# Performance work log

Hardware: AMD Instinct MI355X
Metric: run time of the kernel (lower is better)

The kernel has to match this reference:

```python
import jax, jax.numpy as jnp
import numpy as np

N = 100000   # nodes per type
E = 500000   # edges per edge type
HID = 128    # hidden_channels
H = 4        # heads
D = HID // H # head dim = 32
L = 2        # layers
T = 2        # node types: 0=user, 1=item
R = 2        # edge types: 0=user->item, 1=item->user


def setup_inputs() -> dict:
    key = jax.random.key(0)
    ks = jax.random.split(key, 16)
    s = jnp.float32(0.05)
    f32 = jnp.float32
    return {
        "x_user": jax.random.normal(ks[0], (N, HID), f32),
        "x_item": jax.random.normal(ks[1], (N, HID), f32),
        "W_in": jax.random.normal(ks[2], (T, HID, HID), f32) * s,
        "b_in": jnp.zeros((T, HID), f32),
        "Wk": jax.random.normal(ks[3], (L, T, HID, HID), f32) * s,
        "bk": jnp.zeros((L, T, HID), f32),
        "Wq": jax.random.normal(ks[4], (L, T, HID, HID), f32) * s,
        "bq": jnp.zeros((L, T, HID), f32),
        "Wv": jax.random.normal(ks[5], (L, T, HID, HID), f32) * s,
        "bv": jnp.zeros((L, T, HID), f32),
        "a_rel": jax.random.normal(ks[6], (L, R, H, D, D), f32) * s,
        "m_rel": jax.random.normal(ks[7], (L, R, H, D, D), f32) * s,
        "p_rel": jnp.ones((L, R, H), f32),
        "Wo": jax.random.normal(ks[8], (L, T, HID, HID), f32) * s,
        "bo": jnp.zeros((L, T, HID), f32),
        "skip": jnp.zeros((L, T), f32),
        "edge_ui": jax.random.randint(ks[9], (2, E), 0, N, dtype=jnp.int32),
        "edge_iu": jax.random.randint(ks[10], (2, E), 0, N, dtype=jnp.int32),
    }


def _seg_softmax(logits, seg, n):
    # numerically stable softmax over edges grouped by destination node
    m = jax.ops.segment_max(logits, seg, num_segments=n)            # [N,H]
    m = jnp.where(jnp.isfinite(m), m, jnp.float32(0.0))
    e = jnp.exp(logits - m[seg])                                    # [E,H]
    z = jax.ops.segment_sum(e, seg, num_segments=n)                 # [N,H]
    return e / (z[seg] + jnp.float32(1e-16))


def reference(x_user, x_item, W_in, b_in, Wk, bk, Wq, bq, Wv, bv,
              a_rel, m_rel, p_rel, Wo, bo, skip, edge_ui, edge_iu):
    scale = jnp.float32(1.0 / np.sqrt(D))
    # per-node-type input linear + relu (lin_dict)
    h = [jax.nn.relu(x_user @ W_in[0] + b_in[0]),
         jax.nn.relu(x_item @ W_in[1] + b_in[1])]
    # (edge_type_id, src_type, dst_type, edge_index)
    etypes = [(0, 0, 1, edge_ui), (1, 1, 0, edge_iu)]
    for l in range(L):
        k = [(h[t] @ Wk[l, t] + bk[l, t]).reshape(N, H, D) for t in range(T)]
        q = [(h[t] @ Wq[l, t] + bq[l, t]).reshape(N, H, D) for t in range(T)]
        v = [(h[t] @ Wv[l, t] + bv[l, t]).reshape(N, H, D) for t in range(T)]
        agg = [jnp.zeros((N, H, D), h[0].dtype) for _ in range(T)]
        for r, st, dt, e in etypes:
            src, dst = e[0], e[1]
            # relation-specific transforms applied on node table (N < E)
            k_r = jnp.einsum('nhd,hde->nhe', k[st], a_rel[l, r])
            v_r = jnp.einsum('nhd,hde->nhe', v[st], m_rel[l, r])
            logits = jnp.sum(q[dt][dst] * k_r[src], axis=-1) * p_rel[l, r] * scale  # [E,H]
            alpha = _seg_softmax(logits, dst, N)                                    # [E,H]
            msg = alpha[:, :, None] * v_r[src]                                      # [E,H,D]
            agg[dt] = agg[dt] + jax.ops.segment_sum(msg, dst, num_segments=N)
        h_new = []
        for t in range(T):
            out = agg[t].reshape(N, HID)
            a = jax.nn.gelu(out, approximate=False) @ Wo[l, t] + bo[l, t]
            beta = jax.nn.sigmoid(skip[l, t])
            hn = beta * a + (1.0 - beta) * h[t]
            if l > 0:  # model-level residual (i > 0 in torch code)
                hn = hn + h[t]
            h_new.append(hn)
        h = h_new
    return jnp.stack(h)  # [T, N, HID]
```

## Files before the change

kernel.cpp:

```cpp
#include <hip/hip_runtime.h>
#include <stdint.h>
#include <stdio.h>

#define NN 100000
#define NE 500000
#define HID 128
#define NH 4
#define HD 32
#define LL 2
#define SCANB 1024
#define NB ((NN + SCANB - 1) / SCANB)

typedef unsigned short u16;
typedef unsigned char u8;
typedef unsigned int u32;
typedef __attribute__((ext_vector_type(8))) short bfrag;
typedef __attribute__((ext_vector_type(4))) float f32x4;
typedef __attribute__((ext_vector_type(2))) float f32x2;

__device__ __forceinline__ float b2f(u32 lo16) {
  union { u32 u; float f; } c; c.u = lo16; return c.f;
}
__device__ __forceinline__ u16 f2b(float f) {
  union { float f; u32 u; } c; c.f = f;
  u32 u = c.u;
  u32 r = (u + 0x7FFFu + ((u >> 16) & 1u)) >> 16;
  return (u16)r;
}
__device__ __forceinline__ float geluf(float x) {
  return 0.5f * x * (1.0f + erff(x * 0.70710678118654752f));
}
__device__ __forceinline__ void up8(uint4 a, float* f) {
  f[0] = b2f(a.x << 16); f[1] = b2f(a.x & 0xFFFF0000u);
  f[2] = b2f(a.y << 16); f[3] = b2f(a.y & 0xFFFF0000u);
  f[4] = b2f(a.z << 16); f[5] = b2f(a.z & 0xFFFF0000u);
  f[6] = b2f(a.w << 16); f[7] = b2f(a.w & 0xFFFF0000u);
}
__device__ __forceinline__ float dot32(uint4 a, uint4 b, const float* qv) {
  u32 w[8] = {a.x, a.y, a.z, a.w, b.x, b.y, b.z, b.w};
  float s = 0.f;
#pragma unroll
  for (int j = 0; j < 8; ++j) {
    f32x2 p0 = __builtin_amdgcn_cvt_pk_f32_fp8(w[j], false);
    f32x2 p1 = __builtin_amdgcn_cvt_pk_f32_fp8(w[j], true);
    s += qv[4 * j] * p0.x + qv[4 * j + 1] * p0.y + qv[4 * j + 2] * p1.x + qv[4 * j + 3] * p1.y;
  }
  return s;
}
__device__ __forceinline__ void acc32(uint4 a, uint4 b, float ev, float* acc) {
  u32 w[8] = {a.x, a.y, a.z, a.w, b.x, b.y, b.z, b.w};
#pragma unroll
  for (int j = 0; j < 8; ++j) {
    f32x2 p0 = __builtin_amdgcn_cvt_pk_f32_fp8(w[j], false);
    f32x2 p1 = __builtin_amdgcn_cvt_pk_f32_fp8(w[j], true);
    acc[4 * j] += ev * p0.x; acc[4 * j + 1] += ev * p0.y;
    acc[4 * j + 2] += ev * p1.x; acc[4 * j + 3] += ev * p1.y;
  }
}

__global__ __launch_bounds__(256) void csr_count(const int* __restrict__ e0,
                                                 const int* __restrict__ e1,
                                                 int* __restrict__ deg,
                                                 int* __restrict__ hist) {
  if (blockIdx.x == 0 && blockIdx.y == 0 && threadIdx.x < 128) hist[threadIdx.x] = 0;
  int r = blockIdx.y;
  const int* edges = r ? e1 : e0;
  int e = blockIdx.x * 256 + threadIdx.x;
  if (e < NE) atomicAdd(&deg[(size_t)r * NN + edges[NE + e]], 1);
}

__global__ __launch_bounds__(SCANB) void scan1(const int* __restrict__ deg,
                                               int* __restrict__ rp,
                                               int* __restrict__ bsum,
                                               int* __restrict__ hist) {
  __shared__ int ls[SCANB];
  __shared__ int lh[64];
  int r = blockIdx.y;
  int t = threadIdx.x;
  int g = blockIdx.x * SCANB + t;
  int v = (g < NN) ? deg[(size_t)r * NN + g] : 0;
  ls[t] = v;
  if (t < 64) lh[t] = 0;
  __syncthreads();
  if (g < NN) atomicAdd(&lh[v < 63 ? v : 63], 1);
#pragma unroll
  for (int off = 1; off < SCANB; off <<= 1) {
    int u = (t >= off) ? ls[t - off] : 0;
    __syncthreads();
    ls[t] += u;
    __syncthreads();
  }
  if (g < NN) rp[(size_t)r * (NN + 1) + g] = ls[t] - v;
  if (t == SCANB - 1) bsum[r * NB + blockIdx.x] = ls[t];
  if (t < 64 && lh[t]) atomicAdd(&hist[r * 64 + t], lh[t]);
}

__global__ __launch_bounds__(128) void scan2(const int* __restrict__ bsum,
                                             int* __restrict__ boff,
                                             const int* __restrict__ hist,
                                             int* __restrict__ hcur) {
  __shared__ int ls[128];
  int r = blockIdx.y;
  int t = threadIdx.x;
  int v = (t < NB) ? bsum[r * NB + t] : 0;
  ls[t] = v;
  __syncthreads();
#pragma unroll
  for (int off = 1; off < 128; off <<= 1) {
    int u = (t >= off) ? ls[t - off] : 0;
    __syncthreads();
    ls[t] += u;
    __syncthreads();
  }
  if (t < NB) boff[r * NB + t] = ls[t] - v;
  __syncthreads();
  int hv = (t < 64) ? hist[r * 64 + t] : 0;
  ls[t] = hv;
  __syncthreads();
#pragma unroll
  for (int off = 1; off < 64; off <<= 1) {
    int u = (t >= off) ? ls[t - off] : 0;
    __syncthreads();
    ls[t] += u;
    __syncthreads();
  }
  if (t < 64) hcur[r * 64 + t] = ls[t] - hv;
}

__global__ __launch_bounds__(SCANB) void scan3(int* __restrict__ rp,
                                               int* __restrict__ cursor,
                                               const int* __restrict__ boff,
                                               const int* __restrict__ deg,
                                               int* __restrict__ hcur,
                                               int* __restrict__ o0,
                                               int* __restrict__ o1) {
  __shared__ int lh[64];
  __shared__ int lbase[64];
  int r = blockIdx.y;
  int* order = r ? o1 : o0;
  int t = threadIdx.x;
  int g = blockIdx.x * SCANB + t;
  if (t < 64) lh[t] = 0;
  int dg = 0;
  if (g < NN) {
    int v = rp[(size_t)r * (NN + 1) + g] + boff[r * NB + blockIdx.x];
    rp[(size_t)r * (NN + 1) + g] = v;
    cursor[(size_t)r * NN + g] = v;
    dg = deg[(size_t)r * NN + g];
    if (dg > 63) dg = 63;
  }
  if (g == 0) rp[(size_t)r * (NN + 1) + NN] = NE;
  __syncthreads();
  int rank = 0;
  if (g < NN) rank = atomicAdd(&lh[dg], 1);
  __syncthreads();
  if (t < 64)
    lbase[t] = lh[t] ? atomicAdd(&hcur[r * 64 + t], lh[t]) : 0;
  __syncthreads();
  if (g < NN) order[lbase[dg] + rank] = g;
}

__global__ __launch_bounds__(256) void csr_fill(const int* __restrict__ e0,
                                                const int* __restrict__ e1,
                                                int* __restrict__ cursor,
                                                int* __restrict__ s0,
                                                int* __restrict__ s1) {
  int r = blockIdx.y;
  const int* edges = r ? e1 : e0;
  int* srcs = r ? s1 : s0;
  int e = blockIdx.x * 256 + threadIdx.x;
  if (e < NE) {
    int pos = atomicAdd(&cursor[(size_t)r * NN + edges[NE + e]], 1);
    srcs[pos] = edges[e];
  }
}

__global__ __launch_bounds__(256) void prep_all(
    const float* __restrict__ W_in,
    const float* __restrict__ Wo,
    const float* __restrict__ Wq, const float* __restrict__ bq,
    const float* __restrict__ Wk, const float* __restrict__ bk,
    const float* __restrict__ Wv, const float* __restrict__ bv,
    const float* __restrict__ a_rel, const float* __restrict__ m_rel,
    const float* __restrict__ p_rel,
    u16* __restrict__ winT, u16* __restrict__ woT,
    u16* __restrict__ wqkvT, float* __restrict__ bqkv) {
  const float scale = 0.17677669529663687f;
  int y = blockIdx.y;
  int idx = blockIdx.x * 256 + threadIdx.x;
  if (y < 10) {
    const float* src; u16* dst;
    const float* bsrc = nullptr; float* bdst = nullptr;
    bool useP = false; int m = 0;
    if (y < 2) {
      m = y; src = W_in + (size_t)m * HID * HID; dst = winT + (size_t)m * HID * HID;
    } else if (y < 6) {
      m = y - 2; src = Wo + (size_t)m * HID * HID; dst = woT + (size_t)m * HID * HID;
    } else {
      m = y - 6; src = Wq + (size_t)m * HID * HID;
      dst = wqkvT + (size_t)m * 3 * HID * HID;
      useP = true; bsrc = bq + (size_t)m * HID; bdst = bqkv + (size_t)m * 3 * HID;
    }
    int k = idx >> 7, n = idx & 127;
    float v = src[idx];
    if (useP) {
      int l = m >> 1, t = m & 1;
      v *= p_rel[((l << 1) | (1 - t)) * NH + (n >> 5)] * scale;
    }
    dst[(size_t)n * HID + k] = f2b(v);
    if (bdst != nullptr && blockIdx.x == 0 && threadIdx.x < HID) {
      int col = threadIdx.x;
      int l = m >> 1, t = m & 1;
      bdst[col] = bsrc[col] * p_rel[((l << 1) | (1 - t)) * NH + (col >> 5)] * scale;
    }
  } else {
    int c = y - 10;
    int l = c >> 2, t = (c >> 1) & 1, which = c & 1;
    const float* W  = (which == 0 ? Wk : Wv) + (size_t)(l * 2 + t) * HID * HID;
    const float* b  = (which == 0 ? bk : bv) + (size_t)(l * 2 + t) * HID;
    const float* Ar = (which == 0 ? a_rel : m_rel) + (size_t)(l * 2 + t) * NH * HD * HD;
    u16* Wd = wqkvT + ((size_t)(l * 2 + t) * 3 + 1 + which) * HID * HID;
    float* bd = bqkv + ((size_t)(l * 2 + t) * 3 + 1 + which) * HID;
    int i = idx >> 7, col = idx & 127;
    int h = col >> 5, e = col & 31;
    {
      const float* ap = Ar + h * HD * HD + e;
      const float* wp = W + (size_t)i * HID + h * HD;
      float s = 0.f;
#pragma unroll
      for (int d = 0; d < HD; ++d) s += wp[d] * ap[d * HD];
      Wd[(size_t)col * HID + i] = f2b(s);
    }
    if (blockIdx.x == 0 && threadIdx.x < HID) {
      int col2 = threadIdx.x, h2 = col2 >> 5, e2 = col2 & 31;
      const float* ap = Ar + h2 * HD * HD + e2;
      const float* bp = b + h2 * HD;
      float s = 0.f;
#pragma unroll
      for (int d = 0; d < HD; ++d) s += bp[d] * ap[d * HD];
      bd[col2] = s;
    }
  }
}

__global__ __launch_bounds__(256) void qkv_gemm(
    const u16* __restrict__ h0, const u16* __restrict__ h1,
    const u16* __restrict__ WT,
    const float* __restrict__ bias,
    u16* __restrict__ q0, u16* __restrict__ q1,
    u8* __restrict__ k0, u8* __restrict__ k1,
    u8* __restrict__ v0, u8* __restrict__ v1, int gb) {
  __shared__ __align__(16) u16 sW[2][HID * HID];
  const int t = blockIdx.x >= gb;
  const int bx = t ? blockIdx.x - gb : blockIdx.x;
  const u16* A = t ? h1 : h0;
  const u16* Wg = WT + (size_t)t * 3 * HID * HID;
  const float* bs = bias + (size_t)t * 3 * HID;
  u16* Oq = t ? q1 : q0;
  u8* Ok = t ? k1 : k0;
  u8* Ov = t ? v1 : v0;

  const int lane = threadIdx.x & 63;
  const int wid = threadIdx.x >> 6;
  const int l16 = lane & 15, g = lane >> 4;
  const int rbase = bx * 128 + wid * 32;

  auto stageW = [&](int m, int buf) {
    const u16* Wm = Wg + (size_t)m * HID * HID;
#pragma unroll
    for (int j = 0; j < 8; ++j) {
      int ins = wid * 8 + j;
      int o16 = ins * 64 + lane;
      int row = o16 >> 4, ch = o16 & 15;
      const u16* src = Wm + (size_t)row * HID + ((ch ^ (row & 7)) << 3);
      u16* dst = &sW[buf][0] + (size_t)ins * 512;
      __builtin_amdgcn_global_load_lds(
          (const __attribute__((address_space(1))) unsigned int*)src,
          (__attribute__((address_space(3))) unsigned int*)dst, 16, 0, 0);
    }
  };

  bfrag af[2][4];
#pragma unroll
  for (int rt = 0; rt < 2; ++rt) {
    int row = rbase + rt * 16 + l16;
    int rl = row < NN ? row : NN - 1;
    const bfrag* ap = (const bfrag*)(A + (size_t)rl * HID);
#pragma unroll
    for (int ks = 0; ks < 4; ++ks) af[rt][ks] = ap[ks * 4 + g];
  }

  stageW(0, 0);
  __syncthreads();

  const int rr = threadIdx.x >> 1, half = threadIdx.x & 1;
  const int grow = bx * 128 + rr;

#pragma unroll
  for (int m = 0; m < 3; ++m) {
    if (m + 1 < 3) stageW(m + 1, (m + 1) & 1);
    f32x4 acc[2][8];
#pragma unroll
    for (int rt = 0; rt < 2; ++rt)
#pragma unroll
      for (int ct = 0; ct < 8; ++ct) acc[rt][ct] = (f32x4){0.f, 0.f, 0.f, 0.f};
#pragma unroll
    for (int ct = 0; ct < 8; ++ct) {
      int row = ct * 16 + l16;
      bfrag wf[4];
#pragma unroll
      for (int ks = 0; ks < 4; ++ks)
        wf[ks] = *(const bfrag*)&sW[m & 1][(size_t)row * HID +
                                           (((ks * 4 + g) ^ (row & 7)) << 3)];
#pragma unroll
      for (int ks = 0; ks < 4; ++ks)
#pragma unroll
        for (int rt = 0; rt < 2; ++rt)
          acc[rt][ct] = __builtin_amdgcn_mfma_f32_16x16x32_bf16(wf[ks], af[rt][ks],
                                                                acc[rt][ct], 0, 0, 0);
    }
    __syncthreads();
    u16* tile = &sW[m & 1][0];
    u8* t8 = (u8*)tile;
#pragma unroll
    for (int rt = 0; rt < 2; ++rt) {
      int r = wid * 32 + rt * 16 + l16;
#pragma unroll
      for (int ct = 0; ct < 8; ++ct) {
        int nc = ct * 16 + g * 4;
        const float4 bb = *(const float4*)(bs + m * HID + nc);
        float o0 = acc[rt][ct][0] + bb.x;
        float o1 = acc[rt][ct][1] + bb.y;
        float o2 = acc[rt][ct][2] + bb.z;
        float o3 = acc[rt][ct][3] + bb.w;
        if (m == 0) {
          u32 lo = (u32)f2b(o0) | ((u32)f2b(o1) << 16);
          u32 hi = (u32)f2b(o2) | ((u32)f2b(o3) << 16);
          int sg = ((nc >> 3) ^ (r & 7));
          *(uint2*)&tile[(size_t)r * HID + sg * 8 + (nc & 7)] = make_uint2(lo, hi);
        } else {
          u32 pk = __builtin_amdgcn_cvt_pk_fp8_f32(o0, o1, 0u, false);
          pk = __builtin_amdgcn_cvt_pk_fp8_f32(o2, o3, pk, true);
          int sg = ((nc >> 4) ^ (r & 7));
          *(u32*)&t8[(size_t)r * HID + sg * 16 + (nc & 15)] = pk;
        }
      }
    }
    __syncthreads();
    if (grow < NN) {
      if (m == 0) {
#pragma unroll
        for (int i = 0; i < 8; ++i) {
          int gg = half * 8 + i;
          uint4 d = *(const uint4*)&tile[(size_t)rr * HID + ((gg ^ (rr & 7)) * 8)];
          *(uint4*)(Oq + (size_t)grow * HID + gg * 8) = d;
        }
      } else {
        u8* O8 = (m == 1) ? Ok : Ov;
#pragma unroll
        for (int i = 0; i < 4; ++i) {
          int gg = half * 4 + i;
          uint4 d = *(const uint4*)&t8[(size_t)rr * HID + ((gg ^ (rr & 7)) * 16)];
          *(uint4*)(O8 + (size_t)grow * HID + gg * 16) = d;
        }
      }
    }
    if (m + 1 < 3) __syncthreads();
  }
}

template <int NMAT, bool RELU, bool SKIP, bool FP8KV, bool AF32>
__global__ __launch_bounds__(256) void mfgemm(
    const void* __restrict__ A0, const void* __restrict__ A1, int M, int gb,
    const u16* __restrict__ WT, size_t wtStride,
    const float* __restrict__ bias, size_t biasStride,
    u16* __restrict__ O00, u16* __restrict__ O01, u16* __restrict__ O02,
    u16* __restrict__ O10, u16* __restrict__ O11, u16* __restrict__ O12,
    float* __restrict__ Of0, float* __restrict__ Of1,
    const u16* __restrict__ hp0, const u16* __restrict__ hp1,
    const float* __restrict__ skipP, int resflag) {
  __shared__ __align__(16) u16 sW[HID * HID];
  const int t = blockIdx.x >= gb;
  const int bx = t ? blockIdx.x - gb : blockIdx.x;
  const void* A = t ? A1 : A0;
  const u16* Wg = WT + (size_t)t * wtStride;
  const float* bs = bias + (size_t)t * biasStride;
  u16* Ob = t ? O10 : O00;
  float* Of = t ? Of1 : Of0;
  const u16* hprev = t ? hp1 : hp0;

  const int lane = threadIdx.x & 63;
  const int wid = threadIdx.x >> 6;
  const int l16 = lane & 15, g = lane >> 4;
  const int rbase = bx * 128 + wid * 32;

  float beta = 0.f;
  if (SKIP) beta = 1.f / (1.f + __expf(-skipP[t]));

  {
    const u16* Wm = Wg;
#pragma unroll
    for (int j = 0; j < 8; ++j) {
      int ins = wid * 8 + j;
      int o16 = ins * 64 + lane;
      int row = o16 >> 4, ch = o16 & 15;
      const u16* src = Wm + (size_t)row * HID + ((ch ^ (row & 7)) << 3);
      u16* dst = sW + (size_t)ins * 512;
      __builtin_amdgcn_global_load_lds(
          (const __attribute__((address_space(1))) unsigned int*)src,
          (__attribute__((address_space(3))) unsigned int*)dst, 16, 0, 0);
    }
  }

  bfrag af[2][4];
  int rowA[2];
#pragma unroll
  for (int rt = 0; rt < 2; ++rt) {
    int row = rbase + rt * 16 + l16;
    rowA[rt] = row;
    int rl = row < M ? row : M - 1;
    if (AF32) {
      const float* apf = (const float*)A + (size_t)rl * HID;
#pragma unroll
      for (int ks = 0; ks < 4; ++ks) {
        float4 u0 = *(const float4*)(apf + (ks * 4 + g) * 8);
        float4 u1 = *(const float4*)(apf + (ks * 4 + g) * 8 + 4);
        union { u16 s[8]; bfrag b; } pk;
        pk.s[0] = f2b(u0.x); pk.s[1] = f2b(u0.y); pk.s[2] = f2b(u0.z); pk.s[3] = f2b(u0.w);
        pk.s[4] = f2b(u1.x); pk.s[5] = f2b(u1.y); pk.s[6] = f2b(u1.z); pk.s[7] = f2b(u1.w);
        af[rt][ks] = pk.b;
      }
    } else {
      const bfrag* ap = (const bfrag*)A + (size_t)rl * (HID / 8);
#pragma unroll
      for (int ks = 0; ks < 4; ++ks) af[rt][ks] = ap[ks * 4 + g];
    }
  }

  __syncthreads();

  f32x4 acc[2][8];
#pragma unroll
  for (int rt = 0; rt < 2; ++rt)
#pragma unroll
    for (int ct = 0; ct < 8; ++ct) acc[rt][ct] = (f32x4){0.f, 0.f, 0.f, 0.f};
#pragma unroll
  for (int ct = 0; ct < 8; ++ct) {
    int row = ct * 16 + l16;
    bfrag wf[4];
#pragma unroll
    for (int ks = 0; ks < 4; ++ks)
      wf[ks] = *(const bfrag*)&sW[(size_t)row * HID + (((ks * 4 + g) ^ (row & 7)) << 3)];
#pragma unroll
    for (int ks = 0; ks < 4; ++ks)
#pragma unroll
      for (int rt = 0; rt < 2; ++rt)
        acc[rt][ct] = __builtin_amdgcn_mfma_f32_16x16x32_bf16(wf[ks], af[rt][ks],
                                                              acc[rt][ct], 0, 0, 0);
  }

  if (Ob != nullptr) {
    __syncthreads();
#pragma unroll
    for (int rt = 0; rt < 2; ++rt) {
      int r = wid * 32 + rt * 16 + l16;
      int row = rowA[rt];
      int rl = row < M ? row : M - 1;
#pragma unroll
      for (int ct = 0; ct < 8; ++ct) {
        int nc = ct * 16 + g * 4;
        const float4 bb = *(const float4*)(bs + nc);
        float o0 = acc[rt][ct][0] + bb.x;
        float o1 = acc[rt][ct][1] + bb.y;
        float o2 = acc[rt][ct][2] + bb.z;
        float o3 = acc[rt][ct][3] + bb.w;
        if (RELU) {
          o0 = fmaxf(o0, 0.f); o1 = fmaxf(o1, 0.f);
          o2 = fmaxf(o2, 0.f); o3 = fmaxf(o3, 0.f);
        }
        if (SKIP) {
          uint2 hh2 = *(const uint2*)(hprev + (size_t)rl * HID + nc);
          float h0 = b2f(hh2.x << 16), h1 = b2f(hh2.x & 0xFFFF0000u);
          float h2 = b2f(hh2.y << 16), h3 = b2f(hh2.y & 0xFFFF0000u);
          o0 = beta * o0 + (1.f - beta) * h0;
          o1 = beta * o1 + (1.f - beta) * h1;
          o2 = beta * o2 + (1.f - beta) * h2;
          o3 = beta * o3 + (1.f - beta) * h3;
          if (resflag) { o0 += h0; o1 += h1; o2 += h2; o3 += h3; }
        }
        u32 lo = (u32)f2b(o0) | ((u32)f2b(o1) << 16);
        u32 hi = (u32)f2b(o2) | ((u32)f2b(o3) << 16);
        int sg = ((nc >> 3) ^ (r & 7));
        *(uint2*)&sW[(size_t)r * HID + sg * 8 + (nc & 7)] = make_uint2(lo, hi);
      }
    }
    __syncthreads();
    int rr = threadIdx.x >> 1, half = threadIdx.x & 1;
    int grow = bx * 128 + rr;
    if (grow < M) {
#pragma unroll
      for (int i = 0; i < 8; ++i) {
        int gg = half * 8 + i;
        uint4 d = *(const uint4*)&sW[(size_t)rr * HID + ((gg ^ (rr & 7)) * 8)];
        *(uint4*)(Ob + (size_t)grow * HID + gg * 8) = d;
      }
    }
  } else {
#pragma unroll
    for (int rt = 0; rt < 2; ++rt) {
      int row = rowA[rt];
      if (row >= M) continue;
#pragma unroll
      for (int ct = 0; ct < 8; ++ct) {
        int nc = ct * 16 + g * 4;
        const float4 bb = *(const float4*)(bs + nc);
        float o0 = acc[rt][ct][0] + bb.x;
        float o1 = acc[rt][ct][1] + bb.y;
        float o2 = acc[rt][ct][2] + bb.z;
        float o3 = acc[rt][ct][3] + bb.w;
        if (RELU) {
          o0 = fmaxf(o0, 0.f); o1 = fmaxf(o1, 0.f);
          o2 = fmaxf(o2, 0.f); o3 = fmaxf(o3, 0.f);
        }
        if (SKIP) {
          uint2 hh2 = *(const uint2*)(hprev + (size_t)row * HID + nc);
          float h0 = b2f(hh2.x << 16), h1 = b2f(hh2.x & 0xFFFF0000u);
          float h2 = b2f(hh2.y << 16), h3 = b2f(hh2.y & 0xFFFF0000u);
          o0 = beta * o0 + (1.f - beta) * h0;
          o1 = beta * o1 + (1.f - beta) * h1;
          o2 = beta * o2 + (1.f - beta) * h2;
          o3 = beta * o3 + (1.f - beta) * h3;
          if (resflag) { o0 += h0; o1 += h1; o2 += h2; o3 += h3; }
        }
        *(float4*)(Of + (size_t)row * HID + nc) = make_float4(o0, o1, o2, o3);
      }
    }
  }
}

__global__ __launch_bounds__(256) void agg_csr(
    const int* __restrict__ rp0, const int* __restrict__ ss0, const int* __restrict__ od0,
    const u16* __restrict__ q0, const u8* __restrict__ k0,
    const u8* __restrict__ v0, u16* __restrict__ o0,
    const int* __restrict__ rp1, const int* __restrict__ ss1, const int* __restrict__ od1,
    const u16* __restrict__ q1, const u8* __restrict__ k1,
    const u8* __restrict__ v1, u16* __restrict__ o1, int agb) {
  const int r = blockIdx.x >= agb;
  const int bx = r ? blockIdx.x - agb : blockIdx.x;
  int i = bx * 256 + threadIdx.x;
  if (i >= NN * NH) return;
  const int* rowptr = r ? rp1 : rp0;
  const int* srcs = r ? ss1 : ss0;
  const int* order = r ? od1 : od0;
  const u16* qT = r ? q1 : q0;
  const u8* kT = r ? k1 : k0;
  const u8* vT = r ? v1 : v0;
  u16* aggb = r ? o1 : o0;

  int dst = order[i >> 2], h = i & 3;
  float qv[HD];
  {
    const uint4* qp = (const uint4*)(qT + (size_t)dst * HID + h * HD);
#pragma unroll
    for (int j = 0; j < 4; ++j) up8(qp[j], qv + j * 8);
  }
  float acc[HD];
#pragma unroll
  for (int j = 0; j < HD; ++j) acc[j] = 0.f;
  float z = 0.f;
  int b = rowptr[dst], e2 = rowptr[dst + 1];
  int idx = b;
  for (; idx + 2 <= e2; idx += 2) {
    int s0 = srcs[idx], s1 = srcs[idx + 1];
    const uint4* kp0 = (const uint4*)(kT + (size_t)s0 * HID + h * HD);
    const uint4* vp0 = (const uint4*)(vT + (size_t)s0 * HID + h * HD);
    const uint4* kp1 = (const uint4*)(kT + (size_t)s1 * HID + h * HD);
    const uint4* vp1 = (const uint4*)(vT + (size_t)s1 * HID + h * HD);
    uint4 kA = kp0[0], kB = kp0[1];
    uint4 kC = kp1[0], kD = kp1[1];
    uint4 vA = vp0[0], vB = vp0[1];
    uint4 vC = vp1[0], vD = vp1[1];
    float d0 = dot32(kA, kB, qv);
    float d1 = dot32(kC, kD, qv);
    float ev0 = __expf(fminf(d0, 60.f));
    float ev1 = __expf(fminf(d1, 60.f));
    z += ev0 + ev1;
    acc32(vA, vB, ev0, acc);
    acc32(vC, vD, ev1, acc);
  }
  if (idx < e2) {
    int s0 = srcs[idx];
    const uint4* kp0 = (const uint4*)(kT + (size_t)s0 * HID + h * HD);
    const uint4* vp0 = (const uint4*)(vT + (size_t)s0 * HID + h * HD);
    uint4 kA = kp0[0], kB = kp0[1];
    uint4 vA = vp0[0], vB = vp0[1];
    float d0 = dot32(kA, kB, qv);
    float ev0 = __expf(fminf(d0, 60.f));
    z += ev0;
    acc32(vA, vB, ev0, acc);
  }
  float inv = 1.f / (z + 1e-16f);
  u16* ap = aggb + (size_t)dst * HID + h * HD;
  u32 w[16];
#pragma unroll
  for (int j = 0; j < 16; ++j) {
    float a0 = geluf(acc[2 * j] * inv);
    float a1 = geluf(acc[2 * j + 1] * inv);
    w[j] = (u32)f2b(a0) | ((u32)f2b(a1) << 16);
  }
#pragma unroll
  for (int j = 0; j < 4; ++j)
    *(uint4*)(ap + j * 8) = make_uint4(w[4 * j], w[4 * j + 1], w[4 * j + 2], w[4 * j + 3]);
}

extern "C" void kernel_launch(void* const* d_in, const int* in_sizes, int n_in,
                              void* d_out, int out_size, void* d_ws, size_t ws_size,
                              hipStream_t stream) {
  const float* x_user = (const float*)d_in[0];
  const float* x_item = (const float*)d_in[1];
  const float* W_in = (const float*)d_in[2];
  const float* b_in = (const float*)d_in[3];
  const float* Wk = (const float*)d_in[4];
  const float* bk = (const float*)d_in[5];
  const float* Wq = (const float*)d_in[6];
  const float* bq = (const float*)d_in[7];
  const float* Wv = (const float*)d_in[8];
  const float* bv = (const float*)d_in[9];
  const float* a_rel = (const float*)d_in[10];
  const float* m_rel = (const float*)d_in[11];
  const float* p_rel = (const float*)d_in[12];
  const float* Wo = (const float*)d_in[13];
  const float* bo = (const float*)d_in[14];
  const float* skipP = (const float*)d_in[15];
  const int* edge_ui = (const int*)d_in[16];
  const int* edge_iu = (const int*)d_in[17];
  float* out = (float*)d_out;

  char* p = (char*)d_ws;
  auto take = [&](size_t bytes) {
    void* r = (void*)p;
    p += (bytes + 255) & ~(size_t)255;
    return r;
  };
  size_t nodeB = (size_t)NN * HID * sizeof(u16);
  size_t node8 = (size_t)NN * HID;
  u16* hb[2] = {(u16*)take(nodeB), (u16*)take(nodeB)};
  u16* qb[2] = {(u16*)take(nodeB), (u16*)take(nodeB)};
  u8* kb[2] = {(u8*)take(node8), (u8*)take(node8)};
  u8* vb[2] = {(u8*)take(node8), (u8*)take(node8)};
  u16* aggb[2] = {(u16*)take(nodeB), (u16*)take(nodeB)};
  int* deg2   = (int*)take((size_t)2 * NN * 4);
  int* cur2   = (int*)take((size_t)2 * NN * 4);
  int* bsum2  = (int*)take((size_t)2 * NB * 4);
  int* boff2  = (int*)take((size_t)2 * NB * 4);
  int* hist2  = (int*)take((size_t)2 * 64 * 4);
  int* hcur2  = (int*)take((size_t)2 * 64 * 4);
  int* rp2    = (int*)take((size_t)2 * (NN + 1) * 4);
  int* srcs[2]  = {(int*)take((size_t)NE * 4), (int*)take((size_t)NE * 4)};
  int* order[2] = {(int*)take((size_t)NN * 4), (int*)take((size_t)NN * 4)};
  u16* winT  = (u16*)take((size_t)2 * HID * HID * 2);
  u16* woT   = (u16*)take((size_t)4 * HID * HID * 2);
  u16* wqkvT = (u16*)take((size_t)2 * 2 * 3 * HID * HID * 2);
  float* bqkv = (float*)take((size_t)2 * 2 * 3 * HID * 4);
  size_t used = (size_t)(p - (char*)d_ws);
  if (used > ws_size) {
    fprintf(stderr, "HGT kernel: workspace too small: need %zu, have %zu\n", used, ws_size);
    return;
  }

  const int GB = (NN + 127) / 128;
  const int EB = (NE + 255) / 256;
  dim3 blk(256);

  hipMemsetAsync(deg2, 0, (size_t)2 * NN * 4, stream);
  prep_all<<<dim3(64, 18), blk, 0, stream>>>(W_in, Wo, Wq, bq, Wk, bk, Wv, bv,
                                             a_rel, m_rel, p_rel,
                                             winT, woT, wqkvT, bqkv);
  csr_count<<<dim3(EB, 2), blk, 0, stream>>>(edge_ui, edge_iu, deg2, hist2);
  scan1<<<dim3(NB, 2), SCANB, 0, stream>>>(deg2, rp2, bsum2, hist2);
  scan2<<<dim3(1, 2), 128, 0, stream>>>(bsum2, boff2, hist2, hcur2);
  scan3<<<dim3(NB, 2), SCANB, 0, stream>>>(rp2, cur2, boff2, deg2, hcur2,
                                           order[0], order[1]);
  csr_fill<<<dim3(EB, 2), blk, 0, stream>>>(edge_ui, edge_iu, cur2, srcs[0], srcs[1]);
  int* rowptr[2] = {rp2, rp2 + (NN + 1)};

  mfgemm<1, true, false, false, true><<<2 * GB, blk, 0, stream>>>(
      x_user, x_item, NN, GB, winT, HID * HID, b_in, HID,
      hb[0], nullptr, nullptr, hb[1], nullptr, nullptr,
      nullptr, nullptr, nullptr, nullptr, nullptr, 0);

  const int AGB = (NN * NH + 255) / 256;
  for (int l = 0; l < LL; ++l) {
    qkv_gemm<<<2 * GB, blk, 0, stream>>>(
        hb[0], hb[1],
        wqkvT + (size_t)l * 2 * 3 * HID * HID,
        bqkv + (size_t)l * 2 * 3 * HID,
        qb[0], qb[1], kb[0], kb[1], vb[0], vb[1], GB);
    agg_csr<<<2 * AGB, blk, 0, stream>>>(
        rowptr[0], srcs[0], order[0], qb[1], kb[0], vb[0], aggb[1],
        rowptr[1], srcs[1], order[1], qb[0], kb[1], vb[1], aggb[0], AGB);
    if (l == 0) {
      mfgemm<1, false, true, false, false><<<2 * GB, blk, 0, stream>>>(
          aggb[0], aggb[1], NN, GB,
          woT, HID * HID, bo, HID,
          hb[0], nullptr, nullptr, hb[1], nullptr, nullptr,
          nullptr, nullptr, hb[0], hb[1], skipP, 0);
    } else {
      mfgemm<1, false, true, false, false><<<2 * GB, blk, 0, stream>>>(
          aggb[0], aggb[1], NN, GB,
          woT + (size_t)2 * HID * HID, HID * HID, bo + 2 * HID, HID,
          nullptr, nullptr, nullptr, nullptr, nullptr, nullptr,
          out, out + (size_t)NN * HID, hb[0], hb[1], skipP + 2, 1);
    }
  }
}
```

Measured before the change: 492.7 us.

## Fuse input/output projection GEMM with following QKV GEMM in one kernel

Merges the preceding single-matrix GEMM (input lin+relu, or layer-0 output projection with skip blend) with the QKV projection into one kernel. The intermediate h tile stays in LDS and is reused directly as the A operand, saving one launch per layer and the reload of h from global memory. Shared memory grows to three 32KB weight buffers, which may reduce occupancy. The hb buffer is still written out for the later skip connection.

Result: slower. 512.4 us (+4.0%).

```diff
diff --git a/kernel.cpp b/kernel.cpp
--- a/kernel.cpp
+++ b/kernel.cpp
@@ -243,62 +243,87 @@
   }
 }
 
-__global__ __launch_bounds__(256) void qkv_gemm(
-    const u16* __restrict__ h0, const u16* __restrict__ h1,
-    const u16* __restrict__ WT,
-    const float* __restrict__ bias,
+template <bool FIRSTX>
+__global__ __launch_bounds__(256) void fused_gemm(
+    const void* __restrict__ A0, const void* __restrict__ A1, int gb,
+    const u16* __restrict__ WfT,
+    const float* __restrict__ bf,
+    const u16* __restrict__ WqkvT,
+    const float* __restrict__ bqkv,
+    u16* __restrict__ hb0, u16* __restrict__ hb1,
     u16* __restrict__ q0, u16* __restrict__ q1,
     u8* __restrict__ k0, u8* __restrict__ k1,
-    u8* __restrict__ v0, u8* __restrict__ v1, int gb) {
-  __shared__ __align__(16) u16 sW[2][HID * HID];
+    u8* __restrict__ v0, u8* __restrict__ v1,
+    const float* __restrict__ skipP) {
+  __shared__ __align__(16) u16 sB[3][HID * HID];
   const int t = blockIdx.x >= gb;
   const int bx = t ? blockIdx.x - gb : blockIdx.x;
-  const u16* A = t ? h1 : h0;
-  const u16* Wg = WT + (size_t)t * 3 * HID * HID;
-  const float* bs = bias + (size_t)t * 3 * HID;
+  const void* A = t ? A1 : A0;
+  u16* Oh = t ? hb1 : hb0;
+  const u16* hprev = Oh;
   u16* Oq = t ? q1 : q0;
   u8* Ok = t ? k1 : k0;
   u8* Ov = t ? v1 : v0;
+  const u16* Wqkv = WqkvT + (size_t)t * 3 * HID * HID;
+  const float* bsq = bqkv + (size_t)t * 3 * HID;
 
   const int lane = threadIdx.x & 63;
   const int wid = threadIdx.x >> 6;
   const int l16 = lane & 15, g = lane >> 4;
   const int rbase = bx * 128 + wid * 32;
 
-  auto stageW = [&](int m, int buf) {
-    const u16* Wm = Wg + (size_t)m * HID * HID;
+  auto stage = [&](const u16* Wm, int buf) {
 #pragma unroll
     for (int j = 0; j < 8; ++j) {
       int ins = wid * 8 + j;
       int o16 = ins * 64 + lane;
       int row = o16 >> 4, ch = o16 & 15;
       const u16* src = Wm + (size_t)row * HID + ((ch ^ (row & 7)) << 3);
-      u16* dst = &sW[buf][0] + (size_t)ins * 512;
+      u16* dst = &sB[buf][0] + (size_t)ins * 512;
       __builtin_amdgcn_global_load_lds(
           (const __attribute__((address_space(1))) unsigned int*)src,
           (__attribute__((address_space(3))) unsigned int*)dst, 16, 0, 0);
     }
   };
 
+  stage(WfT + (size_t)t * HID * HID, 0);
+  stage(Wqkv, 1);
+  stage(Wqkv + (size_t)HID * HID, 2);
+
+  float beta = 0.f;
+  if (!FIRSTX) beta = 1.f / (1.f + __expf(-skipP[t]));
+
   bfrag af[2][4];
+  int rowA[2];
 #pragma unroll
   for (int rt = 0; rt < 2; ++rt) {
     int row = rbase + rt * 16 + l16;
+    rowA[rt] = row;
     int rl = row < NN ? row : NN - 1;
-    const bfrag* ap = (const bfrag*)(A + (size_t)rl * HID);
-#pragma unroll
-    for (int ks = 0; ks < 4; ++ks) af[rt][ks] = ap[ks * 4 + g];
-  }
-
-  stageW(0, 0);
-  __syncthreads();
-
+    if (FIRSTX) {
+      const float* apf = (const float*)A + (size_t)rl * HID;
+#pragma unroll
+      for (int ks = 0; ks < 4; ++ks) {
+        float4 u0 = *(const float4*)(apf + (ks * 4 + g) * 8);
+        float4 u1 = *(const float4*)(apf + (ks * 4 + g) * 8 + 4);
+        union { u16 s[8]; bfrag b; } pk;
+        pk.s[0] = f2b(u0.x); pk.s[1] = f2b(u0.y); pk.s[2] = f2b(u0.z); pk.s[3] = f2b(u0.w);
+        pk.s[4] = f2b(u1.x); pk.s[5] = f2b(u1.y); pk.s[6] = f2b(u1.z); pk.s[7] = f2b(u1.w);
+        af[rt][ks] = pk.b;
+      }
+    } else {
+      const bfrag* ap = (const bfrag*)A + (size_t)rl * (HID / 8);
+#pragma unroll
+      for (int ks = 0; ks < 4; ++ks) af[rt][ks] = ap[ks * 4 + g];
+    }
+  }
+  __syncthreads();
+
+  const float* bsf = bf + (size_t)t * HID;
   const int rr = threadIdx.x >> 1, half = threadIdx.x & 1;
   const int grow = bx * 128 + rr;
 
-#pragma unroll
-  for (int m = 0; m < 3; ++m) {
-    if (m + 1 < 3) stageW(m + 1, (m + 1) & 1);
+  {
     f32x4 acc[2][8];
 #pragma unroll
     for (int rt = 0; rt < 2; ++rt)
@@ -310,8 +335,7 @@
       bfrag wf[4];
 #pragma unroll
       for (int ks = 0; ks < 4; ++ks)
-        wf[ks] = *(const bfrag*)&sW[m & 1][(size_t)row * HID +
-                                           (((ks * 4 + g) ^ (row & 7)) << 3)];
+        wf[ks] = *(const bfrag*)&sB[0][(size_t)row * HID + (((ks * 4 + g) ^ (row & 7)) << 3)];
 #pragma unroll
       for (int ks = 0; ks < 4; ++ks)
 #pragma unroll
@@ -320,15 +344,91 @@
                                                                 acc[rt][ct], 0, 0, 0);
     }
     __syncthreads();
-    u16* tile = &sW[m & 1][0];
-    u8* t8 = (u8*)tile;
 #pragma unroll
     for (int rt = 0; rt < 2; ++rt) {
       int r = wid * 32 + rt * 16 + l16;
+      int rl = rowA[rt] < NN ? rowA[rt] : NN - 1;
 #pragma unroll
       for (int ct = 0; ct < 8; ++ct) {
         int nc = ct * 16 + g * 4;
-        const float4 bb = *(const float4*)(bs + m * HID + nc);
+        const float4 bb = *(const float4*)(bsf + nc);
+        float o0 = acc[rt][ct][0] + bb.x;
+        float o1 = acc[rt][ct][1] + bb.y;
+        float o2 = acc[rt][ct][2] + bb.z;
+        float o3 = acc[rt][ct][3] + bb.w;
+        if (FIRSTX) {
+          o0 = fmaxf(o0, 0.f); o1 = fmaxf(o1, 0.f);
+          o2 = fmaxf(o2, 0.f); o3 = fmaxf(o3, 0.f);
+        } else {
+          uint2 hh2 = *(const uint2*)(hprev + (size_t)rl * HID + nc);
+          float h0 = b2f(hh2.x << 16), h1 = b2f(hh2.x & 0xFFFF0000u);
+          float h2 = b2f(hh2.y << 16), h3 = b2f(hh2.y & 0xFFFF0000u);
+          o0 = beta * o0 + (1.f - beta) * h0;
+          o1 = beta * o1 + (1.f - beta) * h1;
+          o2 = beta * o2 + (1.f - beta) * h2;
+          o3 = beta * o3 + (1.f - beta) * h3;
+        }
+        u32 lo = (u32)f2b(o0) | ((u32)f2b(o1) << 16);
+        u32 hi = (u32)f2b(o2) | ((u32)f2b(o3) << 16);
+        int sg = ((nc >> 3) ^ (r & 7));
+        *(uint2*)&sB[0][(size_t)r * HID + sg * 8 + (nc & 7)] = make_uint2(lo, hi);
+      }
+    }
+    __syncthreads();
+  }
+
+  if (grow < NN) {
+#pragma unroll
+    for (int i = 0; i < 8; ++i) {
+      int gg = half * 8 + i;
+      uint4 d = *(const uint4*)&sB[0][(size_t)rr * HID + ((gg ^ (rr & 7)) * 8)];
+      *(uint4*)(Oh + (size_t)grow * HID + gg * 8) = d;
+    }
+  }
+#pragma unroll
+  for (int rt = 0; rt < 2; ++rt) {
+    int r = wid * 32 + rt * 16 + l16;
+#pragma unroll
+    for (int ks = 0; ks < 4; ++ks) {
+      int gg = ks * 4 + g;
+      af[rt][ks] = *(const bfrag*)&sB[0][(size_t)r * HID + ((gg ^ (r & 7)) << 3)];
+    }
+  }
+  __syncthreads();
+  stage(Wqkv + (size_t)2 * HID * HID, 0);
+
+#pragma unroll
+  for (int m = 0; m < 3; ++m) {
+    const int wb = (m == 0) ? 1 : (m == 1) ? 2 : 0;
+    f32x4 acc[2][8];
+#pragma unroll
+    for (int rt = 0; rt < 2; ++rt)
+#pragma unroll
+      for (int ct = 0; ct < 8; ++ct) acc[rt][ct] = (f32x4){0.f, 0.f, 0.f, 0.f};
+#pragma unroll
+    for (int ct = 0; ct < 8; ++ct) {
+      int row = ct * 16 + l16;
+      bfrag wf[4];
+#pragma unroll
+      for (int ks = 0; ks < 4; ++ks)
+        wf[ks] = *(const bfrag*)&sB[wb][(size_t)row * HID + (((ks * 4 + g) ^ (row & 7)) << 3)];
+#pragma unroll
+      for (int ks = 0; ks < 4; ++ks)
+#pragma unroll
+        for (int rt = 0; rt < 2; ++rt)
+          acc[rt][ct] = __builtin_amdgcn_mfma_f32_16x16x32_bf16(wf[ks], af[rt][ks],
+                                                                acc[rt][ct], 0, 0, 0);
+    }
+    __syncthreads();
+    u16* tile = &sB[wb][0];
+    u8* t8 = (u8*)tile;
+#pragma unroll
+    for (int rt = 0; rt < 2; ++rt) {
+      int r = wid * 32 + rt * 16 + l16;
+#pragma unroll
+      for (int ct = 0; ct < 8; ++ct) {
+        int nc = ct * 16 + g * 4;
+        const float4 bb = *(const float4*)(bsq + m * HID + nc);
         float o0 = acc[rt][ct][0] + bb.x;
         float o1 = acc[rt][ct][1] + bb.y;
         float o2 = acc[rt][ct][2] + bb.z;
@@ -369,23 +469,18 @@
   }
 }
 
-template <int NMAT, bool RELU, bool SKIP, bool FP8KV, bool AF32>
-__global__ __launch_bounds__(256) void mfgemm(
-    const void* __restrict__ A0, const void* __restrict__ A1, int M, int gb,
-    const u16* __restrict__ WT, size_t wtStride,
-    const float* __restrict__ bias, size_t biasStride,
-    u16* __restrict__ O00, u16* __restrict__ O01, u16* __restrict__ O02,
-    u16* __restrict__ O10, u16* __restrict__ O11, u16* __restrict__ O12,
+__global__ __launch_bounds__(256) void out_final(
+    const u16* __restrict__ A0, const u16* __restrict__ A1, int gb,
+    const u16* __restrict__ WT, const float* __restrict__ bias,
     float* __restrict__ Of0, float* __restrict__ Of1,
     const u16* __restrict__ hp0, const u16* __restrict__ hp1,
-    const float* __restrict__ skipP, int resflag) {
+    const float* __restrict__ skipP) {
   __shared__ __align__(16) u16 sW[HID * HID];
   const int t = blockIdx.x >= gb;
   const int bx = t ? blockIdx.x - gb : blockIdx.x;
-  const void* A = t ? A1 : A0;
-  const u16* Wg = WT + (size_t)t * wtStride;
-  const float* bs = bias + (size_t)t * biasStride;
-  u16* Ob = t ? O10 : O00;
+  const u16* A = t ? A1 : A0;
+  const u16* Wg = WT + (size_t)t * HID * HID;
+  const float* bs = bias + (size_t)t * HID;
   float* Of = t ? Of1 : Of0;
   const u16* hprev = t ? hp1 : hp0;
 
@@ -394,22 +489,18 @@
   const int l16 = lane & 15, g = lane >> 4;
   const int rbase = bx * 128 + wid * 32;
 
-  float beta = 0.f;
-  if (SKIP) beta = 1.f / (1.f + __expf(-skipP[t]));
-
-  {
-    const u16* Wm = Wg;
-#pragma unroll
-    for (int j = 0; j < 8; ++j) {
-      int ins = wid * 8 + j;
-      int o16 = ins * 64 + lane;
-      int row = o16 >> 4, ch = o16 & 15;
-      const u16* src = Wm + (size_t)row * HID + ((ch ^ (row & 7)) << 3);
-      u16* dst = sW + (size_t)ins * 512;
-      __builtin_amdgcn_global_load_lds(
-          (const __attribute__((address_space(1))) unsigned int*)src,
-          (__attribute__((address_space(3))) unsigned int*)dst, 16, 0, 0);
-    }
+  float beta = 1.f / (1.f + __expf(-skipP[t]));
+
+#pragma unroll
+  for (int j = 0; j < 8; ++j) {
+    int ins = wid * 8 + j;
+    int o16 = ins * 64 + lane;
+    int row = o16 >> 4, ch = o16 & 15;
+    const u16* src = Wg + (size_t)row * HID + ((ch ^ (row & 7)) << 3);
+    u16* dst = sW + (size_t)ins * 512;
+    __builtin_amdgcn_global_load_lds(
+        (const __attribute__((address_space(1))) unsigned int*)src,
+        (__attribute__((address_space(3))) unsigned int*)dst, 16, 0, 0);
   }
 
   bfrag af[2][4];
@@ -418,25 +509,11 @@
   for (int rt = 0; rt < 2; ++rt) {
     int row = rbase + rt * 16 + l16;
     rowA[rt] = row;
-    int rl = row < M ? row : M - 1;
-    if (AF32) {
-      const float* apf = (const float*)A + (size_t)rl * HID;
-#pragma unroll
-      for (int ks = 0; ks < 4; ++ks) {
-        float4 u0 = *(const float4*)(apf + (ks * 4 + g) * 8);
-        float4 u1 = *(const float4*)(apf + (ks * 4 + g) * 8 + 4);
-        union { u16 s[8]; bfrag b; } pk;
-        pk.s[0] = f2b(u0.x); pk.s[1] = f2b(u0.y); pk.s[2] = f2b(u0.z); pk.s[3] = f2b(u0.w);
-        pk.s[4] = f2b(u1.x); pk.s[5] = f2b(u1.y); pk.s[6] = f2b(u1.z); pk.s[7] = f2b(u1.w);
-        af[rt][ks] = pk.b;
-      }
-    } else {
-      const bfrag* ap = (const bfrag*)A + (size_t)rl * (HID / 8);
-#pragma unroll
-      for (int ks = 0; ks < 4; ++ks) af[rt][ks] = ap[ks * 4 + g];
-    }
-  }
-
+    int rl = row < NN ? row : NN - 1;
+    const bfrag* ap = (const bfrag*)(A + (size_t)rl * HID);
+#pragma unroll
+    for (int ks = 0; ks < 4; ++ks) af[rt][ks] = ap[ks * 4 + g];
+  }
   __syncthreads();
 
   f32x4 acc[2][8];
@@ -458,82 +535,26 @@
         acc[rt][ct] = __builtin_amdgcn_mfma_f32_16x16x32_bf16(wf[ks], af[rt][ks],
                                                               acc[rt][ct], 0, 0, 0);
   }
-
-  if (Ob != nullptr) {
-    __syncthreads();
-#pragma unroll
-    for (int rt = 0; rt < 2; ++rt) {
-      int r = wid * 32 + rt * 16 + l16;
-      int row = rowA[rt];
-      int rl = row < M ? row : M - 1;
-#pragma unroll
-      for (int ct = 0; ct < 8; ++ct) {
-        int nc = ct * 16 + g * 4;
-        const float4 bb = *(const float4*)(bs + nc);
-        float o0 = acc[rt][ct][0] + bb.x;
-        float o1 = acc[rt][ct][1] + bb.y;
-        float o2 = acc[rt][ct][2] + bb.z;
-        float o3 = acc[rt][ct][3] + bb.w;
-        if (RELU) {
-          o0 = fmaxf(o0, 0.f); o1 = fmaxf(o1, 0.f);
-          o2 = fmaxf(o2, 0.f); o3 = fmaxf(o3, 0.f);
-        }
-        if (SKIP) {
-          uint2 hh2 = *(const uint2*)(hprev + (size_t)rl * HID + nc);
-          float h0 = b2f(hh2.x << 16), h1 = b2f(hh2.x & 0xFFFF0000u);
-          float h2 = b2f(hh2.y << 16), h3 = b2f(hh2.y & 0xFFFF0000u);
-          o0 = beta * o0 + (1.f - beta) * h0;
-          o1 = beta * o1 + (1.f - beta) * h1;
-          o2 = beta * o2 + (1.f - beta) * h2;
-          o3 = beta * o3 + (1.f - beta) * h3;
-          if (resflag) { o0 += h0; o1 += h1; o2 += h2; o3 += h3; }
-        }
-        u32 lo = (u32)f2b(o0) | ((u32)f2b(o1) << 16);
-        u32 hi = (u32)f2b(o2) | ((u32)f2b(o3) << 16);
-        int sg = ((nc >> 3) ^ (r & 7));
-        *(uint2*)&sW[(size_t)r * HID + sg * 8 + (nc & 7)] = make_uint2(lo, hi);
-      }
-    }
-    __syncthreads();
-    int rr = threadIdx.x >> 1, half = threadIdx.x & 1;
-    int grow = bx * 128 + rr;
-    if (grow < M) {
-#pragma unroll
-      for (int i = 0; i < 8; ++i) {
-        int gg = half * 8 + i;
-        uint4 d = *(const uint4*)&sW[(size_t)rr * HID + ((gg ^ (rr & 7)) * 8)];
-        *(uint4*)(Ob + (size_t)grow * HID + gg * 8) = d;
-      }
-    }
-  } else {
-#pragma unroll
-    for (int rt = 0; rt < 2; ++rt) {
-      int row = rowA[rt];
-      if (row >= M) continue;
-#pragma unroll
-      for (int ct = 0; ct < 8; ++ct) {
-        int nc = ct * 16 + g * 4;
-        const float4 bb = *(const float4*)(bs + nc);
-        float o0 = acc[rt][ct][0] + bb.x;
-        float o1 = acc[rt][ct][1] + bb.y;
-        float o2 = acc[rt][ct][2] + bb.z;
-        float o3 = acc[rt][ct][3] + bb.w;
-        if (RELU) {
-          o0 = fmaxf(o0, 0.f); o1 = fmaxf(o1, 0.f);
-          o2 = fmaxf(o2, 0.f); o3 = fmaxf(o3, 0.f);
-        }
-        if (SKIP) {
-          uint2 hh2 = *(const uint2*)(hprev + (size_t)row * HID + nc);
-          float h0 = b2f(hh2.x << 16), h1 = b2f(hh2.x & 0xFFFF0000u);
-          float h2 = b2f(hh2.y << 16), h3 = b2f(hh2.y & 0xFFFF0000u);
-          o0 = beta * o0 + (1.f - beta) * h0;
-          o1 = beta * o1 + (1.f - beta) * h1;
-          o2 = beta * o2 + (1.f - beta) * h2;
-          o3 = beta * o3 + (1.f - beta) * h3;
-          if (resflag) { o0 += h0; o1 += h1; o2 += h2; o3 += h3; }
-        }
-        *(float4*)(Of + (size_t)row * HID + nc) = make_float4(o0, o1, o2, o3);
-      }
+#pragma unroll
+  for (int rt = 0; rt < 2; ++rt) {
+    int row = rowA[rt];
+    if (row >= NN) continue;
+#pragma unroll
+    for (int ct = 0; ct < 8; ++ct) {
+      int nc = ct * 16 + g * 4;
+      const float4 bb = *(const float4*)(bs + nc);
+      float o0 = acc[rt][ct][0] + bb.x;
+      float o1 = acc[rt][ct][1] + bb.y;
+      float o2 = acc[rt][ct][2] + bb.z;
+      float o3 = acc[rt][ct][3] + bb.w;
+      uint2 hh2 = *(const uint2*)(hprev + (size_t)row * HID + nc);
+      float h0 = b2f(hh2.x << 16), h1 = b2f(hh2.x & 0xFFFF0000u);
+      float h2 = b2f(hh2.y << 16), h3 = b2f(hh2.y & 0xFFFF0000u);
+      o0 = beta * o0 + (1.f - beta) * h0 + h0;
+      o1 = beta * o1 + (1.f - beta) * h1 + h1;
+      o2 = beta * o2 + (1.f - beta) * h2 + h2;
+      o3 = beta * o3 + (1.f - beta) * h3 + h3;
+      *(float4*)(Of + (size_t)row * HID + nc) = make_float4(o0, o1, o2, o3);
     }
   }
 }
@@ -684,33 +705,25 @@
   csr_fill<<<dim3(EB, 2), blk, 0, stream>>>(edge_ui, edge_iu, cur2, srcs[0], srcs[1]);
   int* rowptr[2] = {rp2, rp2 + (NN + 1)};
 
-  mfgemm<1, true, false, false, true><<<2 * GB, blk, 0, stream>>>(
-      x_user, x_item, NN, GB, winT, HID * HID, b_in, HID,
-      hb[0], nullptr, nullptr, hb[1], nullptr, nullptr,
-      nullptr, nullptr, nullptr, nullptr, nullptr, 0);
-
   const int AGB = (NN * NH + 255) / 256;
-  for (int l = 0; l < LL; ++l) {
-    qkv_gemm<<<2 * GB, blk, 0, stream>>>(
-        hb[0], hb[1],
-        wqkvT + (size_t)l * 2 * 3 * HID * HID,
-        bqkv + (size_t)l * 2 * 3 * HID,
-        qb[0], qb[1], kb[0], kb[1], vb[0], vb[1], GB);
-    agg_csr<<<2 * AGB, blk, 0, stream>>>(
-        rowptr[0], srcs[0], order[0], qb[1], kb[0], vb[0], aggb[1],
-        rowptr[1], srcs[1], order[1], qb[0], kb[1], vb[1], aggb[0], AGB);
-    if (l == 0) {
-      mfgemm<1, false, true, false, false><<<2 * GB, blk, 0, stream>>>(
-          aggb[0], aggb[1], NN, GB,
-          woT, HID * HID, bo, HID,
-          hb[0], nullptr, nullptr, hb[1], nullptr, nullptr,
-          nullptr, nullptr, hb[0], hb[1], skipP, 0);
-    } else {
-      mfgemm<1, false, true, false, false><<<2 * GB, blk, 0, stream>>>(
-          aggb[0], aggb[1], NN, GB,
-          woT + (size_t)2 * HID * HID, HID * HID, bo + 2 * HID, HID,
-          nullptr, nullptr, nullptr, nullptr, nullptr, nullptr,
-          out, out + (size_t)NN * HID, hb[0], hb[1], skipP + 2, 1);
-    }
-  }
-}
+
+  fused_gemm<true><<<2 * GB, blk, 0, stream>>>(
+      x_user, x_item, GB, winT, b_in,
+      wqkvT, bqkv,
+      hb[0], hb[1], qb[0], qb[1], kb[0], kb[1], vb[0], vb[1], nullptr);
+  agg_csr<<<2 * AGB, blk, 0, stream>>>(
+      rowptr[0], srcs[0], order[0], qb[1], kb[0], vb[0], aggb[1],
+      rowptr[1], srcs[1], order[1], qb[0], kb[1], vb[1], aggb[0], AGB);
+
+  fused_gemm<false><<<2 * GB, blk, 0, stream>>>(
+      aggb[0], aggb[1], GB, woT, bo,
+      wqkvT + (size_t)2 * 3 * HID * HID, bqkv + (size_t)2 * 3 * HID,
+      hb[0], hb[1], qb[0], qb[1], kb[0], kb[1], vb[0], vb[1], skipP);
+  agg_csr<<<2 * AGB, blk, 0, stream>>>(
+      rowptr[0], srcs[0], order[0], qb[1], kb[0], vb[0], aggb[1],
+      rowptr[1], srcs[1], order[1], qb[0], kb[1], vb[1], aggb[0], AGB);
+  out_final<<<2 * GB, blk, 0, stream>>>(
+      aggb[0], aggb[1], GB,
+      woT + (size_t)2 * HID * HID, bo + 2 * HID,
+      out, out + (size_t)NN * HID, hb[0], hb[1], skipP + 2);
+}
```
